# Kernel tuning notes

Measured on AMD Instinct MI355X. Metric: run time of the kernel, lower is better.

The kernel has to match this reference:

```python
import jax, jax.numpy as jnp
import numpy as np

WINDOW = 7
NUM_HEADS = 16
HEAD_DIM = 32  # dim=512 / 16 heads
SCALE = HEAD_DIM ** -0.5


def _relative_position_index(ws: int) -> np.ndarray:
    ch, cw = np.meshgrid(np.arange(ws), np.arange(ws), indexing='ij')
    coords = np.stack([ch, cw]).reshape(2, -1)            # [2, ws*ws]
    rel = coords[:, :, None] - coords[:, None, :]          # [2, N, N]
    rel = rel.transpose(1, 2, 0)                           # [N, N, 2]
    rel[:, :, 0] += ws - 1
    rel[:, :, 1] += ws - 1
    rel[:, :, 0] *= 2 * ws - 1
    return rel.sum(-1)                                     # [N, N]

REL_IDX = jnp.asarray(_relative_position_index(WINDOW))   # [49, 49] int


def setup_inputs() -> dict:
    key = jax.random.key(0)
    ks = jax.random.split(key, 6)
    B, N, C = 2048, WINDOW * WINDOW, NUM_HEADS * HEAD_DIM
    return {
        'hidden_states': jax.random.normal(ks[0], (B, N, C), jnp.float32),
        'attention_mask': jnp.zeros((B, N, N), jnp.float32),
        'qkv_w': jax.random.normal(ks[1], (3 * C, C), jnp.float32) * 0.02,
        'qkv_b': jax.random.normal(ks[2], (3 * C,), jnp.float32) * 0.02,
        'out_w': jax.random.normal(ks[3], (C, C), jnp.float32) * 0.02,
        'out_b': jax.random.normal(ks[4], (C,), jnp.float32) * 0.02,
        'rel_pos_table': jax.random.normal(ks[5], ((2 * WINDOW - 1) ** 2, NUM_HEADS), jnp.float32) * 0.02,
    }


def reference(hidden_states, attention_mask, qkv_w, qkv_b, out_w, out_b, rel_pos_table):
    B, N, C = hidden_states.shape
    H, D = NUM_HEADS, HEAD_DIM
    qkv = hidden_states @ qkv_w.T + qkv_b                  # [B, N, 3C]
    q, k, v = jnp.split(qkv, 3, axis=-1)
    q = q.reshape(B, N, H, D).transpose(0, 2, 1, 3)        # [B, H, N, D]
    k = k.reshape(B, N, H, D).transpose(0, 2, 1, 3)
    v = v.reshape(B, N, H, D).transpose(0, 2, 1, 3)
    attn = jnp.einsum('bhnd,bhmd->bhnm', q, k) * SCALE     # [B, H, N, N]
    # relative position bias: gather [N*N] rows -> [N, N, H] -> [1, H, N, N]
    bias = rel_pos_table[REL_IDX.reshape(-1)].reshape(N, N, H).transpose(2, 0, 1)
    attn = attn + bias[None] + attention_mask[:, None]
    attn = jax.nn.softmax(attn, axis=-1)                   # dropout = identity (eval)
    out = jnp.einsum('bhnm,bhmd->bhnd', attn, v)           # [B, H, N, D]
    out = out.transpose(0, 2, 1, 3).reshape(B, N, C)
    return out @ out_w.T + out_b
```

## Files before the change

### kernel.cpp

```cpp
#include <hip/hip_runtime.h>
#include <hip/hip_bf16.h>

typedef __attribute__((ext_vector_type(8))) __bf16 bf16x8;
typedef __attribute__((ext_vector_type(4))) __bf16 bf16x4;
typedef __attribute__((ext_vector_type(4))) float f32x4;

#define MFMA16(a,b,c) __builtin_amdgcn_mfma_f32_16x16x32_bf16(a,b,c,0,0,0)

__device__ __forceinline__ void gload_lds16(const void* g, void* l) {
  __builtin_amdgcn_global_load_lds(
      (const __attribute__((address_space(1))) void*)g,
      (__attribute__((address_space(3))) void*)l, 16, 0, 0);
}

__device__ __forceinline__ f32x4 max4(f32x4 a, f32x4 b) {
  f32x4 c;
  c[0] = fmaxf(a[0], b[0]); c[1] = fmaxf(a[1], b[1]);
  c[2] = fmaxf(a[2], b[2]); c[3] = fmaxf(a[3], b[3]);
  return c;
}

__global__ void prep_k(const float* __restrict__ qkv_w, const float* __restrict__ out_w,
                       const float* __restrict__ rpt,
                       __bf16* __restrict__ qwb, __bf16* __restrict__ owb,
                       __bf16* __restrict__ biasb)
{
  int i = blockIdx.x * 256 + threadIdx.x;
  if (i < 786432) { qwb[i] = (__bf16)qkv_w[i]; return; }
  i -= 786432;
  if (i < 262144) { owb[i] = (__bf16)out_w[i]; return; }
  i -= 262144;
  if (i < 65536) {
    int hh = i >> 12, qc = i & 4095, qq = qc >> 6, c = qc & 63;
    __bf16 val;
    if (c >= 49)      val = (__bf16)(-30000.0f);
    else if (qq >= 49) val = (__bf16)(0.0f);
    else {
      int dh = qq / 7 - c / 7 + 6;
      int dw = qq % 7 - c % 7 + 6;
      val = (__bf16)rpt[(dh * 13 + dw) * 16 + hh];
    }
    biasb[i] = val;
  }
}

__global__ void cast_k(const float* __restrict__ in, __bf16* __restrict__ outb, int n8)
{
  int i = blockIdx.x * blockDim.x + threadIdx.x;
  int stride = gridDim.x * blockDim.x;
  for (; i < n8; i += stride) {
    const float4* p = (const float4*)in + (size_t)i * 2;
    float4 x = p[0], y = p[1];
    bf16x8 o;
    o[0] = (__bf16)x.x; o[1] = (__bf16)x.y; o[2] = (__bf16)x.z; o[3] = (__bf16)x.w;
    o[4] = (__bf16)y.x; o[5] = (__bf16)y.y; o[6] = (__bf16)y.z; o[7] = (__bf16)y.w;
    ((bf16x8*)outb)[i] = o;
  }
}

template<int EPI>
__global__ __launch_bounds__(512, 2)
void gemm8p(const __bf16* __restrict__ A, const __bf16* __restrict__ Bt,
            const float* __restrict__ bvec, float* __restrict__ outp,
            __bf16* __restrict__ qb, __bf16* __restrict__ kb, __bf16* __restrict__ vb,
            int N, int K)
{
  __shared__ __align__(16) char lds[131072];
  const int tid = threadIdx.x;
  const int wave = tid >> 6, lane = tid & 63;
  const int g = lane >> 4, r = lane & 15;
  const int l8 = lane >> 3, l7 = lane & 7;
  const int wr = wave >> 2, wc = wave & 3;

  const int ntiles = N >> 8;
  const int nper = gridDim.x >> 3;
  const int b2 = (blockIdx.x & 7) * nper + (blockIdx.x >> 3);
  const int m0 = (b2 / ntiles) << 8;
  const int n0 = (b2 % ntiles) << 8;

  const __bf16* Ag = A + (size_t)(m0 + wave * 8 + l8) * K + (l7 ^ l8) * 8;
  const __bf16* Bg = Bt + (size_t)(n0 + wave * 8 + l8) * K + (l7 ^ l8) * 8;
  const size_t c64 = (size_t)64 * K;

  const int swz = r & 7;
  const int ch0 = (g ^ swz) << 4;
  const int ch1 = ((4 + g) ^ swz) << 4;
  const char* Ar = lds + (wr * 128 + r) * 128;
  const char* Br = lds + 32768 + (wc * 64 + r) * 128;

  f32x4 acc[8][4] = {};
  bf16x8 a[4][2], b[4][2];

#pragma unroll
  for (int c = 0; c < 4; ++c) {
    gload_lds16(Ag + c * c64, lds + wave * 1024 + c * 8192);
    gload_lds16(Bg + c * c64, lds + 32768 + wave * 1024 + c * 8192);
  }
#pragma unroll
  for (int c = 0; c < 4; ++c) {
    gload_lds16(Ag + 64 + c * c64, lds + 65536 + wave * 1024 + c * 8192);
    gload_lds16(Bg + 64 + c * c64, lds + 65536 + 32768 + wave * 1024 + c * 8192);
  }

#pragma unroll 1
  for (int kt = 0; kt < 8; ++kt) {
    const int cur = (kt & 1) << 16;
    const char* Ab = Ar + cur;
    const char* Bb = Br + cur;
    if (kt == 7) asm volatile("s_waitcnt vmcnt(0)" ::: "memory");
    else         asm volatile("s_waitcnt vmcnt(8)" ::: "memory");
    __builtin_amdgcn_s_barrier();

#pragma unroll
    for (int mi = 0; mi < 4; ++mi) {
      a[mi][0] = *(const bf16x8*)(Ab + mi * 2048 + ch0);
      a[mi][1] = *(const bf16x8*)(Ab + mi * 2048 + ch1);
    }
#pragma unroll
    for (int ni = 0; ni < 2; ++ni) {
      b[ni][0] = *(const bf16x8*)(Bb + ni * 2048 + ch0);
      b[ni][1] = *(const bf16x8*)(Bb + ni * 2048 + ch1);
    }
    __builtin_amdgcn_s_barrier();
    asm volatile("s_waitcnt lgkmcnt(0)" ::: "memory");
    __builtin_amdgcn_s_setprio(1);
#pragma unroll
    for (int mi = 0; mi < 4; ++mi)
#pragma unroll
      for (int ni = 0; ni < 2; ++ni) {
        acc[mi][ni] = MFMA16(a[mi][0], b[ni][0], acc[mi][ni]);
        acc[mi][ni] = MFMA16(a[mi][1], b[ni][1], acc[mi][ni]);
      }
    __builtin_amdgcn_s_setprio(0);
    __builtin_amdgcn_s_barrier();

#pragma unroll
    for (int ni = 2; ni < 4; ++ni) {
      b[ni][0] = *(const bf16x8*)(Bb + ni * 2048 + ch0);
      b[ni][1] = *(const bf16x8*)(Bb + ni * 2048 + ch1);
    }
    __builtin_amdgcn_s_barrier();
    asm volatile("s_waitcnt lgkmcnt(0)" ::: "memory");
    __builtin_amdgcn_s_setprio(1);
#pragma unroll
    for (int mi = 0; mi < 4; ++mi)
#pragma unroll
      for (int ni = 2; ni < 4; ++ni) {
        acc[mi][ni] = MFMA16(a[mi][0], b[ni][0], acc[mi][ni]);
        acc[mi][ni] = MFMA16(a[mi][1], b[ni][1], acc[mi][ni]);
      }
    __builtin_amdgcn_s_setprio(0);
    __builtin_amdgcn_s_barrier();

#pragma unroll
    for (int mi = 0; mi < 4; ++mi) {
      a[mi][0] = *(const bf16x8*)(Ab + (4 + mi) * 2048 + ch0);
      a[mi][1] = *(const bf16x8*)(Ab + (4 + mi) * 2048 + ch1);
    }
    __builtin_amdgcn_s_barrier();
    asm volatile("s_waitcnt lgkmcnt(0)" ::: "memory");
    __builtin_amdgcn_s_setprio(1);
#pragma unroll
    for (int mi = 0; mi < 4; ++mi)
#pragma unroll
      for (int ni = 2; ni < 4; ++ni) {
        acc[4 + mi][ni] = MFMA16(a[mi][0], b[ni][0], acc[4 + mi][ni]);
        acc[4 + mi][ni] = MFMA16(a[mi][1], b[ni][1], acc[4 + mi][ni]);
      }
    __builtin_amdgcn_s_setprio(0);
    __builtin_amdgcn_s_barrier();

    if (kt < 6) {
      const __bf16* Agk = Ag + (kt + 2) * 64;
      const __bf16* Bgk = Bg + (kt + 2) * 64;
      char* Al = lds + cur + wave * 1024;
      char* Bl = lds + cur + 32768 + wave * 1024;
#pragma unroll
      for (int c = 0; c < 4; ++c) {
        gload_lds16(Agk + c * c64, Al + c * 8192);
        gload_lds16(Bgk + c * c64, Bl + c * 8192);
      }
    }
    __builtin_amdgcn_s_setprio(1);
#pragma unroll
    for (int mi = 0; mi < 4; ++mi)
#pragma unroll
      for (int ni = 0; ni < 2; ++ni) {
        acc[4 + mi][ni] = MFMA16(a[mi][0], b[ni][0], acc[4 + mi][ni]);
        acc[4 + mi][ni] = MFMA16(a[mi][1], b[ni][1], acc[4 + mi][ni]);
      }
    __builtin_amdgcn_s_setprio(0);
    __builtin_amdgcn_s_barrier();
  }

  if (EPI == 1) {
#pragma unroll
    for (int mi = 0; mi < 8; ++mi) {
      int row = m0 + wr * 128 + mi * 16 + g * 4;
#pragma unroll
      for (int ni = 0; ni < 4; ++ni) {
        int col = n0 + wc * 64 + ni * 16 + r;
        float bv = bvec[col];
#pragma unroll
        for (int j = 0; j < 4; ++j)
          outp[(size_t)(row + j) * N + col] = acc[mi][ni][j] + bv;
      }
    }
  } else {
    __bf16* dst; float scl;
    const int which = n0 >> 9;
    if (which == 0)      { dst = qb; scl = 0.17677669529663687f; }
    else if (which == 1) { dst = kb; scl = 1.0f; }
    else                 { dst = vb; scl = 1.0f; }
    float bv[4];
#pragma unroll
    for (int ni = 0; ni < 4; ++ni) bv[ni] = bvec[n0 + wc * 64 + ni * 16 + r];
#pragma unroll
    for (int mi = 0; mi < 8; ++mi) {
#pragma unroll
      for (int j = 0; j < 4; ++j) {
        int m = m0 + wr * 128 + mi * 16 + g * 4 + j;
        int bb = m / 49, t = m - bb * 49;
        __bf16* drow = dst + ((size_t)bb * 16) * 1568 + t * 32;
#pragma unroll
        for (int ni = 0; ni < 4; ++ni) {
          int nl = (n0 + wc * 64 + ni * 16 + r) & 511;
          int hh = nl >> 5, d = nl & 31;
          float val = (acc[mi][ni][j] + bv[ni]) * scl;
          drow[(size_t)hh * 1568 + d] = (__bf16)val;
        }
      }
    }
  }
}

__global__ __launch_bounds__(256, 4)
void attn_k(const __bf16* __restrict__ qb, const __bf16* __restrict__ kb,
            const __bf16* __restrict__ vb, const __bf16* __restrict__ bias_p,
            const float* __restrict__ mask, __bf16* __restrict__ ao)
{
  __shared__ float maskl[64 * 64];
  __shared__ __bf16 Vt[4][32 * 64];
  __shared__ __bf16 Pl[4][16 * 64];
  const int tid = threadIdx.x, wave = tid >> 6, lane = tid & 63;
  const int g = lane >> 4, r = lane & 15;
  const int b = blockIdx.x >> 2, hg = blockIdx.x & 3;
  const int h = hg * 4 + wave;
  const size_t bh = (size_t)b * 16 + h;
  const __bf16* q = qb + bh * 1568;
  const __bf16* k = kb + bh * 1568;
  const __bf16* v = vb + bh * 1568;
  const bf16x8 z8 = {};
  const f32x4 z4 = {};

  bf16x8* vtz = (bf16x8*)Vt[wave];
#pragma unroll
  for (int i = 0; i < 4; ++i) vtz[i * 64 + lane] = z8;

  const float* mb = mask + (size_t)b * 2401;
#pragma unroll
  for (int i = 0; i < 16; ++i) {
    int idx = i * 256 + tid;
    int qq = idx >> 6, c = idx & 63;
    float mv = (qq < 49 && c < 49) ? mb[qq * 49 + c] : 0.0f;
    maskl[qq * 64 + (c ^ ((qq & 7) << 2))] = mv;
  }

  bf16x8 kf[4], qf[4];
#pragma unroll
  for (int i = 0; i < 4; ++i) {
    int row = i * 16 + r;
    kf[i] = (row < 49) ? *(const bf16x8*)(k + row * 32 + g * 8) : z8;
    qf[i] = (row < 49) ? *(const bf16x8*)(q + row * 32 + g * 8) : z8;
  }

  __syncthreads();

  char* vt = (char*)Vt[wave];
#pragma unroll
  for (int i = 0; i < 4; ++i) {
    int idx = i * 64 + lane;
    int t = idx >> 2, d0 = (idx & 3) << 3;
    if (t < 49) {
      bf16x8 vv = *(const bf16x8*)(v + t * 32 + d0);
#pragma unroll
      for (int j = 0; j < 8; ++j) {
        int d = d0 + j;
        *(__bf16*)(vt + d * 128 + ((t * 2) ^ ((d & 7) << 4))) = vv[j];
      }
    }
  }

  bf16x8 vf[2][2];
#pragma unroll
  for (int di = 0; di < 2; ++di) {
    int row = di * 16 + r;
#pragma unroll
    for (int t = 0; t < 2; ++t)
      vf[di][t] = *(const bf16x8*)(vt + row * 128 + (((t * 32 + g * 8) * 2) ^ ((row & 7) << 4)));
  }

  const __bf16* bp = bias_p + h * 4096;
  char* pw = (char*)Pl[wave];
  __bf16* aob = ao + (size_t)b * 25088 + h * 32;
  const int swz = (r & 7) << 4;
  const int mswz = (r & 7) << 2;

#pragma unroll
  for (int qi = 0; qi < 4; ++qi) {
    f32x4 s[4];
#pragma unroll
    for (int mi = 0; mi < 4; ++mi) s[mi] = MFMA16(kf[mi], qf[qi], z4);

    const int qrow = qi * 16 + r;
#pragma unroll
    for (int mi = 0; mi < 4; ++mi) {
      int c0 = mi * 16 + g * 4;
      bf16x4 b4 = *(const bf16x4*)(bp + qrow * 64 + c0);
      f32x4 m4 = *(const f32x4*)(maskl + qrow * 64 + (c0 ^ mswz));
#pragma unroll
      for (int jj = 0; jj < 4; ++jj)
        s[mi][jj] += (float)b4[jj] + m4[jj];
    }
    f32x4 aa = max4(max4(s[0], s[1]), max4(s[2], s[3]));
    float mx = fmaxf(fmaxf(aa[0], aa[1]), fmaxf(aa[2], aa[3]));
    mx = fmaxf(mx, __shfl_xor(mx, 16));
    mx = fmaxf(mx, __shfl_xor(mx, 32));
    float sum = 0.0f;
#pragma unroll
    for (int mi = 0; mi < 4; ++mi) {
#pragma unroll
      for (int jj = 0; jj < 4; ++jj) {
        float e = __expf(s[mi][jj] - mx);
        s[mi][jj] = e;
        sum += e;
      }
    }
    sum += __shfl_xor(sum, 16);
    sum += __shfl_xor(sum, 32);
    const float rinv = 1.0f / sum;

#pragma unroll
    for (int mi = 0; mi < 4; ++mi) {
      bf16x4 w;
#pragma unroll
      for (int jj = 0; jj < 4; ++jj) w[jj] = (__bf16)(s[mi][jj] * rinv);
      *(bf16x4*)(pw + r * 128 + (((mi * 16 + g * 4) * 2) ^ swz)) = w;
    }
    bf16x8 pa0 = *(const bf16x8*)(pw + r * 128 + ((g * 16) ^ swz));
    bf16x8 pa1 = *(const bf16x8*)(pw + r * 128 + ((64 + g * 16) ^ swz));

#pragma unroll
    for (int di = 0; di < 2; ++di) {
      f32x4 o = MFMA16(pa0, vf[di][0], z4);
      o = MFMA16(pa1, vf[di][1], o);
#pragma unroll
      for (int jj = 0; jj < 4; ++jj) {
        int qq = qi * 16 + g * 4 + jj;
        if (qq < 49)
          aob[(size_t)qq * 512 + di * 16 + r] = (__bf16)o[jj];
      }
    }
  }
}

extern "C" void kernel_launch(void* const* d_in, const int* in_sizes, int n_in,
                              void* d_out, int out_size, void* d_ws, size_t ws_size,
                              hipStream_t stream)
{
  const float* hs    = (const float*)d_in[0];
  const float* mask  = (const float*)d_in[1];
  const float* qkv_w = (const float*)d_in[2];
  const float* qkv_b = (const float*)d_in[3];
  const float* out_w = (const float*)d_in[4];
  const float* out_b = (const float*)d_in[5];
  const float* rpt   = (const float*)d_in[6];
  float* out = (float*)d_out;

  char* ws = (char*)d_ws;
  __bf16* hsb  = (__bf16*)(ws);
  __bf16* qb   = (__bf16*)(ws + 102760448);
  __bf16* kb   = (__bf16*)(ws + 205520896);
  __bf16* vb   = (__bf16*)(ws + 308281344);
  __bf16* qwb  = (__bf16*)(ws + 411041792);
  __bf16* owb  = (__bf16*)(ws + 412614656);
  __bf16* biasb= (__bf16*)(ws + 413138944);

  prep_k<<<4352, 256, 0, stream>>>(qkv_w, out_w, rpt, qwb, owb, biasb);
  cast_k<<<2048, 256, 0, stream>>>(hs, hsb, 6422528);
  gemm8p<0><<<2352, 512, 0, stream>>>(hsb, qwb, qkv_b, nullptr, qb, kb, vb,
                                      1536, 512);
  attn_k<<<8192, 256, 0, stream>>>(qb, kb, vb, biasb, mask, hsb);
  gemm8p<1><<<784, 512, 0, stream>>>(hsb, owb, out_b, out, nullptr, nullptr, nullptr,
                                     512, 512);
}
```

Baseline: 523.3 us.

## Replace 256x256 8-wave GEMM with 128x128 4-wave staggered-prefetch GEMM

Both projection GEMMs switch from a 256x256 tile with 8 waves and 128KB LDS to a 128x128 tile with 4 waves and 64KB LDS, quadrupling the grid size. The K-loop issues the next B tile and the A tile two steps ahead right after the fragment reads, removing several barriers per iteration. The smaller tile improves occupancy and wave-level balance across CUs but lowers data reuse per block and raises global/L2 traffic. The QKV epilogue is also reordered to hoist the bias load per column.

```diff
diff --git a/kernel.cpp b/kernel.cpp
--- a/kernel.cpp
+++ b/kernel.cpp
@@ -59,57 +59,56 @@
 }
 
 template<int EPI>
-__global__ __launch_bounds__(512, 2)
-void gemm8p(const __bf16* __restrict__ A, const __bf16* __restrict__ Bt,
+__global__ __launch_bounds__(256, 2)
+void gemm2p(const __bf16* __restrict__ A, const __bf16* __restrict__ Bt,
             const float* __restrict__ bvec, float* __restrict__ outp,
             __bf16* __restrict__ qb, __bf16* __restrict__ kb, __bf16* __restrict__ vb,
             int N, int K)
 {
-  __shared__ __align__(16) char lds[131072];
+  __shared__ __align__(16) char lds[65536];
   const int tid = threadIdx.x;
   const int wave = tid >> 6, lane = tid & 63;
   const int g = lane >> 4, r = lane & 15;
   const int l8 = lane >> 3, l7 = lane & 7;
-  const int wr = wave >> 2, wc = wave & 3;
-
-  const int ntiles = N >> 8;
+  const int wr = wave >> 1, wc = wave & 1;
+
+  const int ntiles = N >> 7;
   const int nper = gridDim.x >> 3;
   const int b2 = (blockIdx.x & 7) * nper + (blockIdx.x >> 3);
-  const int m0 = (b2 / ntiles) << 8;
-  const int n0 = (b2 % ntiles) << 8;
+  const int m0 = (b2 / ntiles) << 7;
+  const int n0 = (b2 % ntiles) << 7;
 
   const __bf16* Ag = A + (size_t)(m0 + wave * 8 + l8) * K + (l7 ^ l8) * 8;
   const __bf16* Bg = Bt + (size_t)(n0 + wave * 8 + l8) * K + (l7 ^ l8) * 8;
-  const size_t c64 = (size_t)64 * K;
-
-  const int swz = r & 7;
-  const int ch0 = (g ^ swz) << 4;
-  const int ch1 = ((4 + g) ^ swz) << 4;
-  const char* Ar = lds + (wr * 128 + r) * 128;
-  const char* Br = lds + 32768 + (wc * 64 + r) * 128;
-
-  f32x4 acc[8][4] = {};
+  const size_t r32 = (size_t)32 * K;
+
+  const int ch0 = (g ^ (r & 7)) << 4;
+  const int ch1 = ((4 + g) ^ (r & 7)) << 4;
+  const char* Arr = lds + (wr * 64 + r) * 128;
+  const char* Brr = lds + 16384 + (wc * 64 + r) * 128;
+
+  f32x4 acc[4][4] = {};
   bf16x8 a[4][2], b[4][2];
 
 #pragma unroll
   for (int c = 0; c < 4; ++c) {
-    gload_lds16(Ag + c * c64, lds + wave * 1024 + c * 8192);
-    gload_lds16(Bg + c * c64, lds + 32768 + wave * 1024 + c * 8192);
-  }
-#pragma unroll
-  for (int c = 0; c < 4; ++c) {
-    gload_lds16(Ag + 64 + c * c64, lds + 65536 + wave * 1024 + c * 8192);
-    gload_lds16(Bg + 64 + c * c64, lds + 65536 + 32768 + wave * 1024 + c * 8192);
-  }
-
+    gload_lds16(Ag + c * r32, lds + c * 4096 + wave * 1024);
+    gload_lds16(Bg + c * r32, lds + 16384 + c * 4096 + wave * 1024);
+  }
+#pragma unroll
+  for (int c = 0; c < 4; ++c)
+    gload_lds16(Ag + 64 + c * r32, lds + 32768 + c * 4096 + wave * 1024);
+
+  const int nkt = K >> 6;
 #pragma unroll 1
-  for (int kt = 0; kt < 8; ++kt) {
-    const int cur = (kt & 1) << 16;
-    const char* Ab = Ar + cur;
-    const char* Bb = Br + cur;
-    if (kt == 7) asm volatile("s_waitcnt vmcnt(0)" ::: "memory");
-    else         asm volatile("s_waitcnt vmcnt(8)" ::: "memory");
+  for (int kt = 0; kt < nkt; ++kt) {
+    const int cur = (kt & 1) << 15;
+    if (kt == nkt - 1) asm volatile("s_waitcnt vmcnt(0)" ::: "memory");
+    else               asm volatile("s_waitcnt vmcnt(4)" ::: "memory");
     __builtin_amdgcn_s_barrier();
+
+    const char* Ab = Arr + cur;
+    const char* Bb = Brr + cur;
 
 #pragma unroll
     for (int mi = 0; mi < 4; ++mi) {
@@ -121,7 +120,12 @@
       b[ni][0] = *(const bf16x8*)(Bb + ni * 2048 + ch0);
       b[ni][1] = *(const bf16x8*)(Bb + ni * 2048 + ch1);
     }
-    __builtin_amdgcn_s_barrier();
+    if (kt + 1 < nkt) {
+      const __bf16* Bgk = Bg + (kt + 1) * 64;
+      char* Bl = lds + (((kt + 1) & 1) << 15) + 16384 + wave * 1024;
+#pragma unroll
+      for (int c = 0; c < 4; ++c) gload_lds16(Bgk + c * r32, Bl + c * 4096);
+    }
     asm volatile("s_waitcnt lgkmcnt(0)" ::: "memory");
     __builtin_amdgcn_s_setprio(1);
 #pragma unroll
@@ -139,7 +143,12 @@
       b[ni][0] = *(const bf16x8*)(Bb + ni * 2048 + ch0);
       b[ni][1] = *(const bf16x8*)(Bb + ni * 2048 + ch1);
     }
-    __builtin_amdgcn_s_barrier();
+    if (kt + 2 < nkt) {
+      const __bf16* Agk = Ag + (kt + 2) * 64;
+      char* Al = lds + cur + wave * 1024;
+#pragma unroll
+      for (int c = 0; c < 4; ++c) gload_lds16(Agk + c * r32, Al + c * 4096);
+    }
     asm volatile("s_waitcnt lgkmcnt(0)" ::: "memory");
     __builtin_amdgcn_s_setprio(1);
 #pragma unroll
@@ -150,53 +159,12 @@
         acc[mi][ni] = MFMA16(a[mi][1], b[ni][1], acc[mi][ni]);
       }
     __builtin_amdgcn_s_setprio(0);
-    __builtin_amdgcn_s_barrier();
-
-#pragma unroll
-    for (int mi = 0; mi < 4; ++mi) {
-      a[mi][0] = *(const bf16x8*)(Ab + (4 + mi) * 2048 + ch0);
-      a[mi][1] = *(const bf16x8*)(Ab + (4 + mi) * 2048 + ch1);
-    }
-    __builtin_amdgcn_s_barrier();
-    asm volatile("s_waitcnt lgkmcnt(0)" ::: "memory");
-    __builtin_amdgcn_s_setprio(1);
-#pragma unroll
-    for (int mi = 0; mi < 4; ++mi)
-#pragma unroll
-      for (int ni = 2; ni < 4; ++ni) {
-        acc[4 + mi][ni] = MFMA16(a[mi][0], b[ni][0], acc[4 + mi][ni]);
-        acc[4 + mi][ni] = MFMA16(a[mi][1], b[ni][1], acc[4 + mi][ni]);
-      }
-    __builtin_amdgcn_s_setprio(0);
-    __builtin_amdgcn_s_barrier();
-
-    if (kt < 6) {
-      const __bf16* Agk = Ag + (kt + 2) * 64;
-      const __bf16* Bgk = Bg + (kt + 2) * 64;
-      char* Al = lds + cur + wave * 1024;
-      char* Bl = lds + cur + 32768 + wave * 1024;
-#pragma unroll
-      for (int c = 0; c < 4; ++c) {
-        gload_lds16(Agk + c * c64, Al + c * 8192);
-        gload_lds16(Bgk + c * c64, Bl + c * 8192);
-      }
-    }
-    __builtin_amdgcn_s_setprio(1);
-#pragma unroll
-    for (int mi = 0; mi < 4; ++mi)
-#pragma unroll
-      for (int ni = 0; ni < 2; ++ni) {
-        acc[4 + mi][ni] = MFMA16(a[mi][0], b[ni][0], acc[4 + mi][ni]);
-        acc[4 + mi][ni] = MFMA16(a[mi][1], b[ni][1], acc[4 + mi][ni]);
-      }
-    __builtin_amdgcn_s_setprio(0);
-    __builtin_amdgcn_s_barrier();
   }
 
   if (EPI == 1) {
 #pragma unroll
-    for (int mi = 0; mi < 8; ++mi) {
-      int row = m0 + wr * 128 + mi * 16 + g * 4;
+    for (int mi = 0; mi < 4; ++mi) {
+      int row = m0 + wr * 64 + mi * 16 + g * 4;
 #pragma unroll
       for (int ni = 0; ni < 4; ++ni) {
         int col = n0 + wc * 64 + ni * 16 + r;
@@ -212,22 +180,20 @@
     if (which == 0)      { dst = qb; scl = 0.17677669529663687f; }
     else if (which == 1) { dst = kb; scl = 1.0f; }
     else                 { dst = vb; scl = 1.0f; }
-    float bv[4];
-#pragma unroll
-    for (int ni = 0; ni < 4; ++ni) bv[ni] = bvec[n0 + wc * 64 + ni * 16 + r];
-#pragma unroll
-    for (int mi = 0; mi < 8; ++mi) {
-#pragma unroll
-      for (int j = 0; j < 4; ++j) {
-        int m = m0 + wr * 128 + mi * 16 + g * 4 + j;
-        int bb = m / 49, t = m - bb * 49;
-        __bf16* drow = dst + ((size_t)bb * 16) * 1568 + t * 32;
-#pragma unroll
-        for (int ni = 0; ni < 4; ++ni) {
-          int nl = (n0 + wc * 64 + ni * 16 + r) & 511;
-          int hh = nl >> 5, d = nl & 31;
-          float val = (acc[mi][ni][j] + bv[ni]) * scl;
-          drow[(size_t)hh * 1568 + d] = (__bf16)val;
+#pragma unroll
+    for (int mi = 0; mi < 4; ++mi) {
+#pragma unroll
+      for (int ni = 0; ni < 4; ++ni) {
+        int n = n0 + wc * 64 + ni * 16 + r;
+        float bv = bvec[n];
+        int nl = n & 511;
+        int hh = nl >> 5, d = nl & 31;
+#pragma unroll
+        for (int j = 0; j < 4; ++j) {
+          int m = m0 + wr * 64 + mi * 16 + g * 4 + j;
+          int bb = m / 49, t = m - bb * 49;
+          float val = (acc[mi][ni][j] + bv) * scl;
+          dst[(((size_t)bb * 16 + hh) * 49 + t) * 32 + d] = (__bf16)val;
         }
       }
     }
@@ -388,9 +354,9 @@
 
   prep_k<<<4352, 256, 0, stream>>>(qkv_w, out_w, rpt, qwb, owb, biasb);
   cast_k<<<2048, 256, 0, stream>>>(hs, hsb, 6422528);
-  gemm8p<0><<<2352, 512, 0, stream>>>(hsb, qwb, qkv_b, nullptr, qb, kb, vb,
+  gemm2p<0><<<9408, 256, 0, stream>>>(hsb, qwb, qkv_b, nullptr, qb, kb, vb,
                                       1536, 512);
   attn_k<<<8192, 256, 0, stream>>>(qb, kb, vb, biasb, mask, hsb);
-  gemm8p<1><<<784, 512, 0, stream>>>(hsb, owb, out_b, out, nullptr, nullptr, nullptr,
-                                     512, 512);
-}
+  gemm2p<1><<<3136, 256, 0, stream>>>(hsb, owb, out_b, out, nullptr, nullptr, nullptr,
+                                      512, 512);
+}
```

Result: slower. 535.8 us (+2.4%).

## Process all 16 heads per attention block with software-prefetched Q/K/V

Applied to the files above, without the earlier changes.

The attention kernel now launches one block per batch window instead of four, and each wave loops over four heads. The mask is loaded into LDS once per window rather than four times, and the next head's Q/K/V is prefetched into registers while the current head's softmax and PV run. This cuts redundant mask traffic and hides global load latency. In exchange there are fewer blocks, more register pressure from the prefetch buffers, and a serialized per-wave head loop. The GEMM edits only inline the wr/wc variables.

```diff
diff --git a/kernel.cpp b/kernel.cpp
--- a/kernel.cpp
+++ b/kernel.cpp
@@ -82,11 +82,10 @@
   const __bf16* Bg = Bt + (size_t)(n0 + wave * 8 + l8) * K + (l7 ^ l8) * 8;
   const size_t c64 = (size_t)64 * K;
 
-  const int swz = r & 7;
-  const int ch0 = (g ^ swz) << 4;
-  const int ch1 = ((4 + g) ^ swz) << 4;
-  const char* Ar = lds + (wr * 128 + r) * 128;
-  const char* Br = lds + 32768 + (wc * 64 + r) * 128;
+  const int ch0 = (g ^ (r & 7)) << 4;
+  const int ch1 = ((4 + g) ^ (r & 7)) << 4;
+  const char* Ar = lds + ((wave >> 2) * 128 + r) * 128;
+  const char* Br = lds + 32768 + ((wave & 3) * 64 + r) * 128;
 
   f32x4 acc[8][4] = {};
   bf16x8 a[4][2], b[4][2];
@@ -196,10 +195,10 @@
   if (EPI == 1) {
 #pragma unroll
     for (int mi = 0; mi < 8; ++mi) {
-      int row = m0 + wr * 128 + mi * 16 + g * 4;
+      int row = m0 + (wave >> 2) * 128 + mi * 16 + g * 4;
 #pragma unroll
       for (int ni = 0; ni < 4; ++ni) {
-        int col = n0 + wc * 64 + ni * 16 + r;
+        int col = n0 + (wave & 3) * 64 + ni * 16 + r;
         float bv = bvec[col];
 #pragma unroll
         for (int j = 0; j < 4; ++j)
@@ -214,17 +213,17 @@
     else                 { dst = vb; scl = 1.0f; }
     float bv[4];
 #pragma unroll
-    for (int ni = 0; ni < 4; ++ni) bv[ni] = bvec[n0 + wc * 64 + ni * 16 + r];
+    for (int ni = 0; ni < 4; ++ni) bv[ni] = bvec[n0 + (wave & 3) * 64 + ni * 16 + r];
 #pragma unroll
     for (int mi = 0; mi < 8; ++mi) {
 #pragma unroll
       for (int j = 0; j < 4; ++j) {
-        int m = m0 + wr * 128 + mi * 16 + g * 4 + j;
+        int m = m0 + (wave >> 2) * 128 + mi * 16 + g * 4 + j;
         int bb = m / 49, t = m - bb * 49;
         __bf16* drow = dst + ((size_t)bb * 16) * 1568 + t * 32;
 #pragma unroll
         for (int ni = 0; ni < 4; ++ni) {
-          int nl = (n0 + wc * 64 + ni * 16 + r) & 511;
+          int nl = (n0 + (wave & 3) * 64 + ni * 16 + r) & 511;
           int hh = nl >> 5, d = nl & 31;
           float val = (acc[mi][ni][j] + bv[ni]) * scl;
           drow[(size_t)hh * 1568 + d] = (__bf16)val;
@@ -244,18 +243,37 @@
   __shared__ __bf16 Pl[4][16 * 64];
   const int tid = threadIdx.x, wave = tid >> 6, lane = tid & 63;
   const int g = lane >> 4, r = lane & 15;
-  const int b = blockIdx.x >> 2, hg = blockIdx.x & 3;
-  const int h = hg * 4 + wave;
-  const size_t bh = (size_t)b * 16 + h;
-  const __bf16* q = qb + bh * 1568;
-  const __bf16* k = kb + bh * 1568;
-  const __bf16* v = vb + bh * 1568;
+  const int b = blockIdx.x;
   const bf16x8 z8 = {};
   const f32x4 z4 = {};
+  const size_t bbase = (size_t)b * 16;
 
   bf16x8* vtz = (bf16x8*)Vt[wave];
 #pragma unroll
   for (int i = 0; i < 4; ++i) vtz[i * 64 + lane] = z8;
+
+  bf16x8 vv[4];
+  int vt_[4], vd0_[4];
+  {
+    const __bf16* v = vb + (bbase + wave) * 1568;
+#pragma unroll
+    for (int i = 0; i < 4; ++i) {
+      int idx = i * 64 + lane;
+      vt_[i] = idx >> 2; vd0_[i] = (idx & 3) << 3;
+      vv[i] = (vt_[i] < 49) ? *(const bf16x8*)(v + vt_[i] * 32 + vd0_[i]) : z8;
+    }
+  }
+  bf16x8 qf[4], kf[4];
+  {
+    const __bf16* q = qb + (bbase + wave) * 1568;
+    const __bf16* k = kb + (bbase + wave) * 1568;
+#pragma unroll
+    for (int i = 0; i < 4; ++i) {
+      int row = i * 16 + r;
+      qf[i] = (row < 49) ? *(const bf16x8*)(q + row * 32 + g * 8) : z8;
+      kf[i] = (row < 49) ? *(const bf16x8*)(k + row * 32 + g * 8) : z8;
+    }
+  }
 
   const float* mb = mask + (size_t)b * 2401;
 #pragma unroll
@@ -265,100 +283,130 @@
     float mv = (qq < 49 && c < 49) ? mb[qq * 49 + c] : 0.0f;
     maskl[qq * 64 + (c ^ ((qq & 7) << 2))] = mv;
   }
-
-  bf16x8 kf[4], qf[4];
-#pragma unroll
-  for (int i = 0; i < 4; ++i) {
-    int row = i * 16 + r;
-    kf[i] = (row < 49) ? *(const bf16x8*)(k + row * 32 + g * 8) : z8;
-    qf[i] = (row < 49) ? *(const bf16x8*)(q + row * 32 + g * 8) : z8;
-  }
-
   __syncthreads();
 
   char* vt = (char*)Vt[wave];
-#pragma unroll
-  for (int i = 0; i < 4; ++i) {
-    int idx = i * 64 + lane;
-    int t = idx >> 2, d0 = (idx & 3) << 3;
-    if (t < 49) {
-      bf16x8 vv = *(const bf16x8*)(v + t * 32 + d0);
-#pragma unroll
-      for (int j = 0; j < 8; ++j) {
-        int d = d0 + j;
-        *(__bf16*)(vt + d * 128 + ((t * 2) ^ ((d & 7) << 4))) = vv[j];
-      }
-    }
-  }
-
-  bf16x8 vf[2][2];
-#pragma unroll
-  for (int di = 0; di < 2; ++di) {
-    int row = di * 16 + r;
-#pragma unroll
-    for (int t = 0; t < 2; ++t)
-      vf[di][t] = *(const bf16x8*)(vt + row * 128 + (((t * 32 + g * 8) * 2) ^ ((row & 7) << 4)));
-  }
-
-  const __bf16* bp = bias_p + h * 4096;
   char* pw = (char*)Pl[wave];
-  __bf16* aob = ao + (size_t)b * 25088 + h * 32;
   const int swz = (r & 7) << 4;
   const int mswz = (r & 7) << 2;
 
 #pragma unroll
-  for (int qi = 0; qi < 4; ++qi) {
-    f32x4 s[4];
-#pragma unroll
-    for (int mi = 0; mi < 4; ++mi) s[mi] = MFMA16(kf[mi], qf[qi], z4);
-
-    const int qrow = qi * 16 + r;
-#pragma unroll
-    for (int mi = 0; mi < 4; ++mi) {
-      int c0 = mi * 16 + g * 4;
-      bf16x4 b4 = *(const bf16x4*)(bp + qrow * 64 + c0);
-      f32x4 m4 = *(const f32x4*)(maskl + qrow * 64 + (c0 ^ mswz));
-#pragma unroll
-      for (int jj = 0; jj < 4; ++jj)
-        s[mi][jj] += (float)b4[jj] + m4[jj];
-    }
-    f32x4 aa = max4(max4(s[0], s[1]), max4(s[2], s[3]));
-    float mx = fmaxf(fmaxf(aa[0], aa[1]), fmaxf(aa[2], aa[3]));
-    mx = fmaxf(mx, __shfl_xor(mx, 16));
-    mx = fmaxf(mx, __shfl_xor(mx, 32));
-    float sum = 0.0f;
-#pragma unroll
-    for (int mi = 0; mi < 4; ++mi) {
-#pragma unroll
-      for (int jj = 0; jj < 4; ++jj) {
-        float e = __expf(s[mi][jj] - mx);
-        s[mi][jj] = e;
-        sum += e;
-      }
-    }
-    sum += __shfl_xor(sum, 16);
-    sum += __shfl_xor(sum, 32);
-    const float rinv = 1.0f / sum;
-
-#pragma unroll
-    for (int mi = 0; mi < 4; ++mi) {
-      bf16x4 w;
-#pragma unroll
-      for (int jj = 0; jj < 4; ++jj) w[jj] = (__bf16)(s[mi][jj] * rinv);
-      *(bf16x4*)(pw + r * 128 + (((mi * 16 + g * 4) * 2) ^ swz)) = w;
-    }
-    bf16x8 pa0 = *(const bf16x8*)(pw + r * 128 + ((g * 16) ^ swz));
-    bf16x8 pa1 = *(const bf16x8*)(pw + r * 128 + ((64 + g * 16) ^ swz));
-
+  for (int i = 0; i < 4; ++i) {
+    if (vt_[i] < 49) {
+#pragma unroll
+      for (int j = 0; j < 8; ++j) {
+        int d = vd0_[i] + j;
+        *(__bf16*)(vt + d * 128 + ((vt_[i] * 2) ^ ((d & 7) << 4))) = vv[i][j];
+      }
+    }
+  }
+
+#pragma unroll
+  for (int hi = 0; hi < 4; ++hi) {
+    const int h = wave + hi * 4;
+    __bf16* aob = ao + (size_t)b * 25088 + h * 32;
+    const __bf16* bp = bias_p + h * 4096;
+
+    bf16x8 vf[2][2];
 #pragma unroll
     for (int di = 0; di < 2; ++di) {
-      f32x4 o = MFMA16(pa0, vf[di][0], z4);
-      o = MFMA16(pa1, vf[di][1], o);
-#pragma unroll
-      for (int jj = 0; jj < 4; ++jj) {
-        int qq = qi * 16 + g * 4 + jj;
-        if (qq < 49)
-          aob[(size_t)qq * 512 + di * 16 + r] = (__bf16)o[jj];
+      int row = di * 16 + r;
+#pragma unroll
+      for (int t = 0; t < 2; ++t)
+        vf[di][t] = *(const bf16x8*)(vt + row * 128 + (((t * 32 + g * 8) * 2) ^ ((row & 7) << 4)));
+    }
+
+    bf16x8 vn[4];
+    if (hi < 3) {
+      const __bf16* v = vb + (bbase + h + 4) * 1568;
+#pragma unroll
+      for (int i = 0; i < 4; ++i)
+        vn[i] = (vt_[i] < 49) ? *(const bf16x8*)(v + vt_[i] * 32 + vd0_[i]) : z8;
+    }
+
+    f32x4 s01[4], s23[4];
+    bf16x8 qn[4], kn[4];
+
+#pragma unroll
+    for (int qi = 0; qi < 4; ++qi) {
+      f32x4 s[4];
+#pragma unroll
+      for (int mi = 0; mi < 4; ++mi) s[mi] = MFMA16(kf[mi], qf[qi], z4);
+
+      if (qi == 3 && hi < 3) {
+        const __bf16* q = qb + (bbase + h + 4) * 1568;
+        const __bf16* k = kb + (bbase + h + 4) * 1568;
+#pragma unroll
+        for (int i = 0; i < 4; ++i) {
+          int row = i * 16 + r;
+          qn[i] = (row < 49) ? *(const bf16x8*)(q + row * 32 + g * 8) : z8;
+          kn[i] = (row < 49) ? *(const bf16x8*)(k + row * 32 + g * 8) : z8;
+        }
+      }
+
+      const int qrow = qi * 16 + r;
+#pragma unroll
+      for (int mi = 0; mi < 4; ++mi) {
+        int c0 = mi * 16 + g * 4;
+        bf16x4 b4 = *(const bf16x4*)(bp + qrow * 64 + c0);
+        f32x4 m4 = *(const f32x4*)(maskl + qrow * 64 + (c0 ^ mswz));
+#pragma unroll
+        for (int jj = 0; jj < 4; ++jj)
+          s[mi][jj] += (float)b4[jj] + m4[jj];
+      }
+      f32x4 aa = max4(max4(s[0], s[1]), max4(s[2], s[3]));
+      float mx = fmaxf(fmaxf(aa[0], aa[1]), fmaxf(aa[2], aa[3]));
+      mx = fmaxf(mx, __shfl_xor(mx, 16));
+      mx = fmaxf(mx, __shfl_xor(mx, 32));
+      float sum = 0.0f;
+#pragma unroll
+      for (int mi = 0; mi < 4; ++mi) {
+#pragma unroll
+        for (int jj = 0; jj < 4; ++jj) {
+          float e = __expf(s[mi][jj] - mx);
+          s[mi][jj] = e;
+          sum += e;
+        }
+      }
+      sum += __shfl_xor(sum, 16);
+      sum += __shfl_xor(sum, 32);
+      const float rinv = 1.0f / sum;
+
+#pragma unroll
+      for (int mi = 0; mi < 4; ++mi) {
+        bf16x4 w;
+#pragma unroll
+        for (int jj = 0; jj < 4; ++jj) w[jj] = (__bf16)(s[mi][jj] * rinv);
+        *(bf16x4*)(pw + r * 128 + (((mi * 16 + g * 4) * 2) ^ swz)) = w;
+      }
+      bf16x8 pa0 = *(const bf16x8*)(pw + r * 128 + ((g * 16) ^ swz));
+      bf16x8 pa1 = *(const bf16x8*)(pw + r * 128 + ((64 + g * 16) ^ swz));
+
+#pragma unroll
+      for (int di = 0; di < 2; ++di) {
+        f32x4 o = MFMA16(pa0, vf[di][0], z4);
+        o = MFMA16(pa1, vf[di][1], o);
+#pragma unroll
+        for (int jj = 0; jj < 4; ++jj) {
+          int qq = qi * 16 + g * 4 + jj;
+          if (qq < 49)
+            aob[(size_t)qq * 512 + di * 16 + r] = (__bf16)o[jj];
+        }
+      }
+    }
+
+    if (hi < 3) {
+#pragma unroll
+      for (int i = 0; i < 4; ++i) { qf[i] = qn[i]; kf[i] = kn[i]; }
+#pragma unroll
+      for (int i = 0; i < 4; ++i) {
+        if (vt_[i] < 49) {
+#pragma unroll
+          for (int j = 0; j < 8; ++j) {
+            int d = vd0_[i] + j;
+            *(__bf16*)(vt + d * 128 + ((vt_[i] * 2) ^ ((d & 7) << 4))) = vn[i][j];
+          }
+        }
       }
     }
   }
@@ -390,7 +438,7 @@
   cast_k<<<2048, 256, 0, stream>>>(hs, hsb, 6422528);
   gemm8p<0><<<2352, 512, 0, stream>>>(hsb, qwb, qkv_b, nullptr, qb, kb, vb,
                                       1536, 512);
-  attn_k<<<8192, 256, 0, stream>>>(qb, kb, vb, biasb, mask, hsb);
+  attn_k<<<2048, 256, 0, stream>>>(qb, kb, vb, biasb, mask, hsb);
   gemm8p<1><<<784, 512, 0, stream>>>(hsb, owb, out_b, out, nullptr, nullptr, nullptr,
                                      512, 512);
 }
```

After: 648.7 us. 24.0% more time.

## Load GEMM A operand directly from global into registers, stage only B in LDS

Applied to the files above, without the earlier changes.

The GEMM now stages only the B (weight) tile in LDS, double-buffered, which halves shared memory to 64 KB. The A fragments are loaded straight from global memory into registers in MFMA layout and software-pipelined one k-step ahead. This drops most barriers and the LDS traffic for A. In exchange, each wave issues uncoalesced 16-byte global loads for A, A rows are re-read by the four column waves, and register pressure rises.

```diff
diff --git a/kernel.cpp b/kernel.cpp
--- a/kernel.cpp
+++ b/kernel.cpp
@@ -60,12 +60,12 @@
 
 template<int EPI>
 __global__ __launch_bounds__(512, 2)
-void gemm8p(const __bf16* __restrict__ A, const __bf16* __restrict__ Bt,
+void gemmha(const __bf16* __restrict__ A, const __bf16* __restrict__ Bt,
             const float* __restrict__ bvec, float* __restrict__ outp,
             __bf16* __restrict__ qb, __bf16* __restrict__ kb, __bf16* __restrict__ vb,
             int N, int K)
 {
-  __shared__ __align__(16) char lds[131072];
+  __shared__ __align__(16) char lds[65536];
   const int tid = threadIdx.x;
   const int wave = tid >> 6, lane = tid & 63;
   const int g = lane >> 4, r = lane & 15;
@@ -78,120 +78,70 @@
   const int m0 = (b2 / ntiles) << 8;
   const int n0 = (b2 % ntiles) << 8;
 
-  const __bf16* Ag = A + (size_t)(m0 + wave * 8 + l8) * K + (l7 ^ l8) * 8;
   const __bf16* Bg = Bt + (size_t)(n0 + wave * 8 + l8) * K + (l7 ^ l8) * 8;
   const size_t c64 = (size_t)64 * K;
+
+  const __bf16* Ag = A + (size_t)(m0 + wr * 128 + r) * K + g * 8;
+  const size_t mstride = (size_t)16 * K;
 
   const int swz = r & 7;
   const int ch0 = (g ^ swz) << 4;
   const int ch1 = ((4 + g) ^ swz) << 4;
-  const char* Ar = lds + (wr * 128 + r) * 128;
-  const char* Br = lds + 32768 + (wc * 64 + r) * 128;
+  const char* Br = lds + (wc * 64 + r) * 128;
 
   f32x4 acc[8][4] = {};
-  bf16x8 a[4][2], b[4][2];
-
-#pragma unroll
-  for (int c = 0; c < 4; ++c) {
-    gload_lds16(Ag + c * c64, lds + wave * 1024 + c * 8192);
-    gload_lds16(Bg + c * c64, lds + 32768 + wave * 1024 + c * 8192);
-  }
-#pragma unroll
-  for (int c = 0; c < 4; ++c) {
-    gload_lds16(Ag + 64 + c * c64, lds + 65536 + wave * 1024 + c * 8192);
-    gload_lds16(Bg + 64 + c * c64, lds + 65536 + 32768 + wave * 1024 + c * 8192);
-  }
+  bf16x8 aP[8], aQ[8], bf[4];
+
+#define STAGEB(T) {                                                            \
+    const __bf16* Bs_ = Bg + (T) * 64;                                         \
+    char* Bl_ = lds + (((T) & 1) << 15) + wave * 1024;                         \
+    _Pragma("unroll")                                                          \
+    for (int c = 0; c < 4; ++c) gload_lds16(Bs_ + c * c64, Bl_ + c * 8192); }
+
+  STAGEB(0);
+#pragma unroll
+  for (int mi = 0; mi < 8; ++mi) aP[mi] = *(const bf16x8*)(Ag + mi * mstride);
 
 #pragma unroll 1
   for (int kt = 0; kt < 8; ++kt) {
-    const int cur = (kt & 1) << 16;
-    const char* Ab = Ar + cur;
-    const char* Bb = Br + cur;
-    if (kt == 7) asm volatile("s_waitcnt vmcnt(0)" ::: "memory");
-    else         asm volatile("s_waitcnt vmcnt(8)" ::: "memory");
+    const int cur = (kt & 1) << 15;
+    asm volatile("s_waitcnt vmcnt(8)" ::: "memory");
     __builtin_amdgcn_s_barrier();
-
-#pragma unroll
-    for (int mi = 0; mi < 4; ++mi) {
-      a[mi][0] = *(const bf16x8*)(Ab + mi * 2048 + ch0);
-      a[mi][1] = *(const bf16x8*)(Ab + mi * 2048 + ch1);
-    }
-#pragma unroll
-    for (int ni = 0; ni < 2; ++ni) {
-      b[ni][0] = *(const bf16x8*)(Bb + ni * 2048 + ch0);
-      b[ni][1] = *(const bf16x8*)(Bb + ni * 2048 + ch1);
-    }
-    __builtin_amdgcn_s_barrier();
-    asm volatile("s_waitcnt lgkmcnt(0)" ::: "memory");
+    if (kt < 7) STAGEB(kt + 1);
+
+#pragma unroll
+    for (int ni = 0; ni < 4; ++ni)
+      bf[ni] = *(const bf16x8*)(Br + cur + ni * 2048 + ch0);
+    {
+      const __bf16* ap = Ag + kt * 64 + 32;
+#pragma unroll
+      for (int mi = 0; mi < 8; ++mi) aQ[mi] = *(const bf16x8*)(ap + mi * mstride);
+    }
     __builtin_amdgcn_s_setprio(1);
 #pragma unroll
-    for (int mi = 0; mi < 4; ++mi)
-#pragma unroll
-      for (int ni = 0; ni < 2; ++ni) {
-        acc[mi][ni] = MFMA16(a[mi][0], b[ni][0], acc[mi][ni]);
-        acc[mi][ni] = MFMA16(a[mi][1], b[ni][1], acc[mi][ni]);
-      }
+    for (int mi = 0; mi < 8; ++mi)
+#pragma unroll
+      for (int ni = 0; ni < 4; ++ni)
+        acc[mi][ni] = MFMA16(aP[mi], bf[ni], acc[mi][ni]);
     __builtin_amdgcn_s_setprio(0);
-    __builtin_amdgcn_s_barrier();
-
-#pragma unroll
-    for (int ni = 2; ni < 4; ++ni) {
-      b[ni][0] = *(const bf16x8*)(Bb + ni * 2048 + ch0);
-      b[ni][1] = *(const bf16x8*)(Bb + ni * 2048 + ch1);
-    }
-    __builtin_amdgcn_s_barrier();
-    asm volatile("s_waitcnt lgkmcnt(0)" ::: "memory");
+
+#pragma unroll
+    for (int ni = 0; ni < 4; ++ni)
+      bf[ni] = *(const bf16x8*)(Br + cur + ni * 2048 + ch1);
+    if (kt < 7) {
+      const __bf16* ap = Ag + (kt + 1) * 64;
+#pragma unroll
+      for (int mi = 0; mi < 8; ++mi) aP[mi] = *(const bf16x8*)(ap + mi * mstride);
+    }
     __builtin_amdgcn_s_setprio(1);
 #pragma unroll
-    for (int mi = 0; mi < 4; ++mi)
-#pragma unroll
-      for (int ni = 2; ni < 4; ++ni) {
-        acc[mi][ni] = MFMA16(a[mi][0], b[ni][0], acc[mi][ni]);
-        acc[mi][ni] = MFMA16(a[mi][1], b[ni][1], acc[mi][ni]);
-      }
+    for (int mi = 0; mi < 8; ++mi)
+#pragma unroll
+      for (int ni = 0; ni < 4; ++ni)
+        acc[mi][ni] = MFMA16(aQ[mi], bf[ni], acc[mi][ni]);
     __builtin_amdgcn_s_setprio(0);
-    __builtin_amdgcn_s_barrier();
-
-#pragma unroll
-    for (int mi = 0; mi < 4; ++mi) {
-      a[mi][0] = *(const bf16x8*)(Ab + (4 + mi) * 2048 + ch0);
-      a[mi][1] = *(const bf16x8*)(Ab + (4 + mi) * 2048 + ch1);
-    }
-    __builtin_amdgcn_s_barrier();
-    asm volatile("s_waitcnt lgkmcnt(0)" ::: "memory");
-    __builtin_amdgcn_s_setprio(1);
-#pragma unroll
-    for (int mi = 0; mi < 4; ++mi)
-#pragma unroll
-      for (int ni = 2; ni < 4; ++ni) {
-        acc[4 + mi][ni] = MFMA16(a[mi][0], b[ni][0], acc[4 + mi][ni]);
-        acc[4 + mi][ni] = MFMA16(a[mi][1], b[ni][1], acc[4 + mi][ni]);
-      }
-    __builtin_amdgcn_s_setprio(0);
-    __builtin_amdgcn_s_barrier();
-
-    if (kt < 6) {
-      const __bf16* Agk = Ag + (kt + 2) * 64;
-      const __bf16* Bgk = Bg + (kt + 2) * 64;
-      char* Al = lds + cur + wave * 1024;
-      char* Bl = lds + cur + 32768 + wave * 1024;
-#pragma unroll
-      for (int c = 0; c < 4; ++c) {
-        gload_lds16(Agk + c * c64, Al + c * 8192);
-        gload_lds16(Bgk + c * c64, Bl + c * 8192);
-      }
-    }
-    __builtin_amdgcn_s_setprio(1);
-#pragma unroll
-    for (int mi = 0; mi < 4; ++mi)
-#pragma unroll
-      for (int ni = 0; ni < 2; ++ni) {
-        acc[4 + mi][ni] = MFMA16(a[mi][0], b[ni][0], acc[4 + mi][ni]);
-        acc[4 + mi][ni] = MFMA16(a[mi][1], b[ni][1], acc[4 + mi][ni]);
-      }
-    __builtin_amdgcn_s_setprio(0);
-    __builtin_amdgcn_s_barrier();
-  }
+  }
+#undef STAGEB
 
   if (EPI == 1) {
 #pragma unroll
@@ -388,9 +338,9 @@
 
   prep_k<<<4352, 256, 0, stream>>>(qkv_w, out_w, rpt, qwb, owb, biasb);
   cast_k<<<2048, 256, 0, stream>>>(hs, hsb, 6422528);
-  gemm8p<0><<<2352, 512, 0, stream>>>(hsb, qwb, qkv_b, nullptr, qb, kb, vb,
+  gemmha<0><<<2352, 512, 0, stream>>>(hsb, qwb, qkv_b, nullptr, qb, kb, vb,
                                       1536, 512);
   attn_k<<<8192, 256, 0, stream>>>(qb, kb, vb, biasb, mask, hsb);
-  gemm8p<1><<<784, 512, 0, stream>>>(hsb, owb, out_b, out, nullptr, nullptr, nullptr,
+  gemmha<1><<<784, 512, 0, stream>>>(hsb, owb, out_b, out, nullptr, nullptr, nullptr,
                                      512, 512);
 }
```

Result: slower. 727.2 us (+39.0%).
